# Performance work log

Hardware: AMD Instinct MI355X
Metric: run time of the kernel (lower is better)

Reference implementation:

```python
import jax, jax.numpy as jnp
import numpy as np

R = 32          # voxel_resolution
GN_GROUPS = 8   # GroupNorm groups used throughout the module


def group_norm(x, scale, bias, groups, eps=1e-5):
    B, C = x.shape[0], x.shape[1]
    spatial = x.shape[2:]
    xg = x.reshape(B, groups, C // groups, -1)
    mu = xg.mean(axis=(2, 3), keepdims=True)
    var = xg.var(axis=(2, 3), keepdims=True)
    xn = ((xg - mu) / jnp.sqrt(var + eps)).reshape((B, C) + spatial)
    sh = (1, C) + (1,) * len(spatial)
    return xn * scale.reshape(sh) + bias.reshape(sh)


def conv3d_same(x, w, b):
    pad = w.shape[-1] // 2
    y = jax.lax.conv_general_dilated(
        x, w, (1, 1, 1), [(pad, pad)] * 3,
        dimension_numbers=('NCDHW', 'OIDHW', 'NCDHW'))
    return y + b.reshape(1, -1, 1, 1, 1)


def _voxelize(coords, features, r):
    # PVCNN Voxelization: center coords, normalize to [0,1], scale to grid,
    # scatter-MEAN point features into a dense [B,C,r,r,r] grid.
    B, C, N = features.shape
    centered = coords - coords.mean(axis=2, keepdims=True)            # [B,3,N]
    norm = jnp.linalg.norm(centered, axis=1, keepdims=True)           # [B,1,N]
    denom = norm.max(axis=2, keepdims=True) * 2.0                     # eps = 0
    nc = centered / denom + 0.5
    nc = jnp.clip(nc * r, 0.0, r - 1.0)                               # float voxel coords
    vi = jnp.round(nc).astype(jnp.int32)                              # [B,3,N]
    flat = (vi[:, 0] * r + vi[:, 1]) * r + vi[:, 2]                   # [B,N]
    seg = (flat + (jnp.arange(B, dtype=jnp.int32) * (r ** 3))[:, None]).reshape(-1)
    feats = features.transpose(0, 2, 1).reshape(B * N, C)
    sums = jax.ops.segment_sum(feats, seg, num_segments=B * r ** 3)
    cnts = jax.ops.segment_sum(jnp.ones((B * N,), feats.dtype), seg,
                               num_segments=B * r ** 3)
    mean = sums / jnp.maximum(cnts, 1.0)[:, None]
    grid = mean.reshape(B, r, r, r, C).transpose(0, 4, 1, 2, 3)       # [B,C,r,r,r]
    return nc, grid


def _trilinear_devoxelize(nc, grid, r):
    # nc [B,3,N] float in [0,r-1]; grid [B,C,r,r,r] -> gather 8 corners + weights
    B, C = grid.shape[0], grid.shape[1]
    lo = jnp.floor(nc)
    frac = nc - lo                                                    # [B,3,N]
    lo_i = lo.astype(jnp.int32)
    hi_i = jnp.minimum(lo_i + 1, r - 1)
    gf = grid.reshape(B, C, r * r * r)
    out = jnp.zeros((B, C, nc.shape[2]), grid.dtype)
    for dx in (0, 1):
        for dy in (0, 1):
            for dz in (0, 1):
                ix = hi_i[:, 0] if dx else lo_i[:, 0]
                iy = hi_i[:, 1] if dy else lo_i[:, 1]
                iz = hi_i[:, 2] if dz else lo_i[:, 2]
                w = ((frac[:, 0] if dx else 1.0 - frac[:, 0]) *
                     (frac[:, 1] if dy else 1.0 - frac[:, 1]) *
                     (frac[:, 2] if dz else 1.0 - frac[:, 2]))        # [B,N]
                idx = (ix * r + iy) * r + iz                          # [B,N]
                g = jnp.take_along_axis(gf, idx[:, None, :], axis=2)  # [B,C,N]
                out = out + g * w[:, None, :]
    return out


def setup_inputs() -> dict:
    key = jax.random.key(0)
    ks = jax.random.split(key, 6)
    B, N, Cin, Cout, K = 4, 65536, 64, 128, 3
    return {
        'coords':   jax.random.normal(ks[0], (B, 3, N), jnp.float32),
        'features': jax.random.normal(ks[1], (B, Cin, N), jnp.float32),
        'conv1_w':  jax.random.normal(ks[2], (Cout, Cin, K, K, K), jnp.float32) * 0.02,
        'conv1_b':  jnp.zeros((Cout,), jnp.float32),
        'gn1_scale': jnp.ones((Cout,), jnp.float32),
        'gn1_bias':  jnp.zeros((Cout,), jnp.float32),
        'conv2_w':  jax.random.normal(ks[3], (Cout, Cout, K, K, K), jnp.float32) * 0.02,
        'conv2_b':  jnp.zeros((Cout,), jnp.float32),
        'gn2_scale': jnp.ones((Cout,), jnp.float32),
        'gn2_bias':  jnp.zeros((Cout,), jnp.float32),
        'point_w':  jax.random.normal(ks[4], (Cout, Cin), jnp.float32) * 0.05,
        'point_b':  jnp.zeros((Cout,), jnp.float32),
        'point_gn_scale': jnp.ones((Cout,), jnp.float32),
        'point_gn_bias':  jnp.zeros((Cout,), jnp.float32),
    }


def reference(coords, features, conv1_w, conv1_b, gn1_scale, gn1_bias,
              conv2_w, conv2_b, gn2_scale, gn2_bias,
              point_w, point_b, point_gn_scale, point_gn_bias):
    nc, grid = _voxelize(coords, features, R)
    # voxel branch: Conv3d -> GN -> SiLU -> (dropout, eval: identity) -> Conv3d -> GN -> SiLU
    h = conv3d_same(grid, conv1_w, conv1_b)
    h = jax.nn.silu(group_norm(h, gn1_scale, gn1_bias, GN_GROUPS))
    h = conv3d_same(h, conv2_w, conv2_b)
    h = jax.nn.silu(group_norm(h, gn2_scale, gn2_bias, GN_GROUPS))
    # point branch: SharedMLP = 1x1 Conv1d -> GN -> SiLU
    p = jnp.einsum('oc,bcn->bon', point_w, features) + point_b[None, :, None]
    p = jax.nn.silu(group_norm(p, point_gn_scale, point_gn_bias, GN_GROUPS))
    vpts = _trilinear_devoxelize(nc, h, R)                            # [B,Cout,N]
    return p + vpts
```

## Files before the change

### kernel.cpp

```cpp
#include <hip/hip_runtime.h>

typedef __attribute__((ext_vector_type(8))) short bf16x8;
typedef __attribute__((ext_vector_type(4))) float f32x4;
typedef __attribute__((ext_vector_type(4))) int i32x4;
typedef __attribute__((ext_vector_type(2))) int i32x2;

#define B_ 4
#define N_ 65536
#define RRR_ 32768
#define PADV_ 39304
#define PPLANE_ 1156

static const size_t OFF_NC     = 0;
static const size_t OFF_VIDX   = 786432;
static const size_t OFF_WT1    = 1048576;
static const size_t OFF_WT2    = 1159168;
static const size_t OFF_C2OUT  = 1380352;
static const size_t OFF_CNT    = 9768960;
static const size_t OFF_GSUM   = 9900032;
static const size_t OFF_GPAD   = 18288640;
static const size_t OFF_ACT1   = 23319552;
static const size_t OFF_GSTATS = 33381376;
static const size_t OFF_BSTATS = 33381568;
static const size_t MEMSET_FLOATS = 33381584 - 9768960;
static const size_t OFF_PBF    = 9900032;

__device__ __forceinline__ ushort f2bf(float x) {
    union { float f; unsigned u; } c; c.f = x;
    unsigned r = c.u + 0x7fffu + ((c.u >> 16) & 1u);
    return (ushort)(r >> 16);
}
__device__ __forceinline__ float bf2f(ushort h) {
    union { unsigned u; float f; } c; c.u = ((unsigned)h) << 16;
    return c.f;
}

__device__ __forceinline__ void gl16(const void* g, void* l) {
    __builtin_amdgcn_global_load_lds(
        (const __attribute__((address_space(1))) unsigned int*)(g),
        (__attribute__((address_space(3))) unsigned int*)(l),
        16, 0, 0);
}

__global__ __launch_bounds__(256) void k_coord_sum(const float* __restrict__ coords,
                                                   float* __restrict__ bstats) {
    int b = blockIdx.y;
    int tid = threadIdx.x;
    const float* cb = coords + (size_t)b * 3 * N_;
    float s0 = 0.f, s1 = 0.f, s2 = 0.f;
    for (int n = blockIdx.x * 256 + tid; n < N_; n += 64 * 256) {
        s0 += cb[n]; s1 += cb[N_ + n]; s2 += cb[2 * N_ + n];
    }
    #pragma unroll
    for (int off = 1; off < 64; off <<= 1) {
        s0 += __shfl_xor(s0, off);
        s1 += __shfl_xor(s1, off);
        s2 += __shfl_xor(s2, off);
    }
    if ((tid & 63) == 0) {
        atomicAdd(&bstats[b * 4 + 0], s0);
        atomicAdd(&bstats[b * 4 + 1], s1);
        atomicAdd(&bstats[b * 4 + 2], s2);
    }
}

__global__ __launch_bounds__(256) void k_coord_max(const float* __restrict__ coords,
                                                   float* __restrict__ bstats) {
    int b = blockIdx.y;
    int tid = threadIdx.x;
    const float invN = 1.0f / (float)N_;
    float m0 = bstats[b * 4 + 0] * invN;
    float m1 = bstats[b * 4 + 1] * invN;
    float m2 = bstats[b * 4 + 2] * invN;
    const float* cb = coords + (size_t)b * 3 * N_;
    float mx = 0.f;
    for (int n = blockIdx.x * 256 + tid; n < N_; n += 64 * 256) {
        float x = cb[n] - m0, y = cb[N_ + n] - m1, z = cb[2 * N_ + n] - m2;
        mx = fmaxf(mx, x * x + y * y + z * z);
    }
    #pragma unroll
    for (int off = 1; off < 64; off <<= 1)
        mx = fmaxf(mx, __shfl_xor(mx, off));
    if ((tid & 63) == 0)
        atomicMax((int*)&bstats[b * 4 + 3], __float_as_int(mx));
}

__global__ __launch_bounds__(256) void k_point_prep(const float* __restrict__ coords,
                                                    const float* __restrict__ bstats,
                                                    float* __restrict__ nc,
                                                    int* __restrict__ vidx,
                                                    float* __restrict__ cnt) {
    int gid = blockIdx.x * 256 + threadIdx.x;
    int b = gid >> 16;
    int n = gid & (N_ - 1);
    const float invN = 1.0f / (float)N_;
    float m[3] = {bstats[b * 4 + 0] * invN, bstats[b * 4 + 1] * invN, bstats[b * 4 + 2] * invN};
    float den = 2.0f * sqrtf(__int_as_float(((const int*)bstats)[b * 4 + 3]));
    const float* cb = coords + (size_t)b * 3 * N_;
    int vi[3];
    #pragma unroll
    for (int d = 0; d < 3; ++d) {
        float cv = cb[(size_t)d * N_ + n];
        float t = (cv - m[d]) / den + 0.5f;
        t *= 32.0f;
        t = fminf(fmaxf(t, 0.0f), 31.0f);
        nc[((size_t)b * 3 + d) * N_ + n] = t;
        vi[d] = (int)rintf(t);
    }
    int flat = (vi[0] * 32 + vi[1]) * 32 + vi[2];
    vidx[(b << 16) + n] = flat;
    atomicAdd(&cnt[(b << 15) + flat], 1.0f);
}

__global__ __launch_bounds__(256) void k_scatter_cl(const float* __restrict__ feats,
                                                    const int* __restrict__ vidx,
                                                    float* __restrict__ gsum) {
    __shared__ float lf[64 * 129];
    __shared__ int sidx[128];
    int tid = threadIdx.x;
    int b = blockIdx.y;
    int n0 = blockIdx.x * 128;
    for (int i = tid; i < 64 * 128; i += 256) {
        int ci = i >> 7, pt = i & 127;
        lf[ci * 129 + pt] = feats[((size_t)(b * 64 + ci)) * N_ + n0 + pt];
    }
    if (tid < 128) sidx[tid] = vidx[(b << 16) + n0 + tid];
    __syncthreads();
    for (int i = tid; i < 64 * 128; i += 256) {
        int ci = i & 63, pt = i >> 6;
        atomicAdd(&gsum[((size_t)(b << 15) + sidx[pt]) * 64 + ci], lf[ci * 129 + pt]);
    }
}

__global__ __launch_bounds__(256) void k_gridmean_cl(const float* __restrict__ gsum,
                                                     const float* __restrict__ cnt,
                                                     ushort* __restrict__ gpad) {
    int idx = blockIdx.x * 256 + threadIdx.x;
    int q = idx & 15;
    int vox = (idx >> 4) & 32767;
    int b = idx >> 19;
    float c = cnt[(b << 15) + vox];
    float inv = 1.0f / fmaxf(c, 1.0f);
    float4 v = *(const float4*)(gsum + (((size_t)(b << 15) + vox) << 6) + q * 4);
    int zz = vox >> 10, yy = (vox >> 5) & 31, xx = vox & 31;
    size_t o = ((size_t)b * PADV_ + (size_t)(zz + 1) * PPLANE_ + (yy + 1) * 34 + (xx + 1)) * 64 + q * 4;
    i32x2 pk;
    ushort* u = (ushort*)&pk;
    u[0] = f2bf(v.x * inv); u[1] = f2bf(v.y * inv);
    u[2] = f2bf(v.z * inv); u[3] = f2bf(v.w * inv);
    *(i32x2*)(gpad + o) = pk;
}

template <int CI>
__global__ __launch_bounds__(256) void k_wtrans(const float* __restrict__ w,
                                                ushort* __restrict__ wt) {
    int idx = blockIdx.x * 256 + threadIdx.x;
    if (idx >= 27 * 128 * CI) return;
    int chin = idx & 31;
    int co = (idx >> 5) & 127;
    int t3 = idx >> 12;
    int tap = t3 % 27;
    int chunk = t3 / 27;
    int ci = chunk * 32 + chin;
    wt[idx] = f2bf(w[((size_t)co * CI + ci) * 27 + tap]);
}

template <int CI, bool PAD_OUT>
__global__ __launch_bounds__(256, 2) void k_conv(const ushort* __restrict__ inp,
                                                 const ushort* __restrict__ wt,
                                                 const float* __restrict__ bias,
                                                 ushort* __restrict__ outp,
                                                 float* __restrict__ gstats,
                                                 int layer) {
    constexpr int NCHUNK = CI / 32;
    __shared__ char lds[65536];
    char* ring = lds + 40960;

    const int bid = blockIdx.x;
    const int wid = (bid & 7) * 128 + (bid >> 3);
    const int yg = wid & 7;
    const int z0 = (wid >> 3) & 31;
    const int b = wid >> 8;
    const int y0 = yg * 4;
    const int tid = threadIdx.x;
    const int w = tid >> 6, l = tid & 63;
    const int lk = l >> 4, lr = l & 15;
    const int wr = w >> 1, wc = w & 1;

    const char* actb = (const char*)(inp + (size_t)b * PADV_ * CI);
    const char* wtb = (const char*)wt;

    int st_glb[10];
    #pragma unroll
    for (int j = 0; j < 10; ++j) {
        int c = j * 64 + (tid >> 2);
        if (c > 611) c = 611;
        int row = c / 34;
        int x = c - row * 34;
        int dz = row / 6, dy = row - dz * 6;
        int gz = z0 + dz, gy = y0 + dy;
        int lq = (tid & 3) ^ ((x >> 1) & 3);
        st_glb[j] = (gz * PPLANE_ + gy * 34 + x) * CI * 2 + lq * 16;
    }
    int bst[2];
    #pragma unroll
    for (int i = 0; i < 2; ++i) {
        int s = tid + i * 256;
        int q = s & 3, co = s >> 2;
        bst[i] = co * 64 + ((q ^ ((co >> 1) & 3)) << 4);
    }
    int aoff[4][3];
    #pragma unroll
    for (int i = 0; i < 4; ++i) {
        int pos = wr * 64 + i * 16 + lr;
        int ly = pos >> 5, x = pos & 31;
        #pragma unroll
        for (int fx = 0; fx < 3; ++fx) {
            int xc = x + fx;
            aoff[i][fx] = (ly * 34 + xc) * 64 + ((lk ^ ((xc >> 1) & 3)) << 4);
        }
    }
    int boff[4];
    #pragma unroll
    for (int n = 0; n < 4; ++n) {
        int co = wc * 64 + n * 16 + lr;
        boff[n] = co * 64 + ((lk ^ ((co >> 1) & 3)) << 4);
    }

    f32x4 acc[4][4];
    #pragma unroll
    for (int i = 0; i < 4; ++i)
        #pragma unroll
        for (int n = 0; n < 4; ++n)
            acc[i][n] = (f32x4){0.f, 0.f, 0.f, 0.f};

    #pragma unroll 1
    for (int chunk = 0; chunk < NCHUNK; ++chunk) {
        const char* srcb = actb + chunk * 64;
        const char* wch = wtb + (size_t)chunk * 27 * 8192;
        #pragma unroll
        for (int j = 0; j < 10; ++j)
            gl16(srcb + st_glb[j], lds + j * 4096 + w * 1024);
        #pragma unroll
        for (int i = 0; i < 2; ++i)
            gl16(wch + bst[i], ring + i * 4096 + w * 1024);
        #pragma unroll
        for (int i = 0; i < 2; ++i)
            gl16(wch + 8192 + bst[i], ring + 8192 + i * 4096 + w * 1024);

        #pragma unroll
        for (int t = 0; t < 27; ++t) {
            __builtin_amdgcn_sched_barrier(0);
            if (t == 26) {
                asm volatile("s_waitcnt vmcnt(0)" ::: "memory");
            } else {
                asm volatile("s_waitcnt vmcnt(2)" ::: "memory");
            }
            __builtin_amdgcn_sched_barrier(0);
            __builtin_amdgcn_s_barrier();
            __builtin_amdgcn_sched_barrier(0);
            const char* rp = ring + (t % 3) * 8192;
            const int fz = t / 9, r9v = t - fz * 9;
            const int fy = r9v / 3, fx = r9v - fy * 3;
            const int drow = (fz * 6 + fy) * 2176;
            bf16x8 af[4], bfr[4];
            #pragma unroll
            for (int i = 0; i < 4; ++i)
                af[i] = *(const bf16x8*)(lds + drow + aoff[i][fx]);
            #pragma unroll
            for (int n = 0; n < 4; ++n)
                bfr[n] = *(const bf16x8*)(rp + boff[n]);
            __builtin_amdgcn_s_setprio(1);
            #pragma unroll
            for (int i = 0; i < 4; ++i)
                #pragma unroll
                for (int n = 0; n < 4; ++n)
                    acc[i][n] = __builtin_amdgcn_mfma_f32_16x16x32_bf16(af[i], bfr[n], acc[i][n], 0, 0, 0);
            __builtin_amdgcn_s_setprio(0);
            __builtin_amdgcn_sched_barrier(0);
            if (t + 2 < 27) {
                const char* wp = wch + (size_t)(t + 2) * 8192;
                char* rw = ring + ((t + 2) % 3) * 8192;
                #pragma unroll
                for (int i = 0; i < 2; ++i)
                    gl16(wp + bst[i], rw + i * 4096 + w * 1024);
            }
            __builtin_amdgcn_sched_barrier(0);
        }
        __builtin_amdgcn_s_barrier();
        __builtin_amdgcn_sched_barrier(0);
    }

    ushort* outs = (ushort*)lds;
    float bb[4];
    #pragma unroll
    for (int n = 0; n < 4; ++n) bb[n] = bias[wc * 64 + n * 16 + lr];
    float sg[4] = {0.f, 0.f, 0.f, 0.f}, sq[4] = {0.f, 0.f, 0.f, 0.f};
    #pragma unroll
    for (int i = 0; i < 4; ++i) {
        int posb = wr * 64 + i * 16 + lk * 4;
        #pragma unroll
        for (int n = 0; n < 4; ++n) {
            int co = wc * 64 + n * 16 + lr;
            #pragma unroll
            for (int r = 0; r < 4; ++r) {
                float v = acc[i][n][r] + bb[n];
                sg[n] += v; sq[n] += v * v;
                outs[(posb + r) * 128 + co] = f2bf(v);
            }
        }
    }
    #pragma unroll
    for (int off = 1; off < 64; off <<= 1) {
        #pragma unroll
        for (int n = 0; n < 4; ++n) {
            sg[n] += __shfl_xor(sg[n], off);
            sq[n] += __shfl_xor(sq[n], off);
        }
    }
    if (l == 0) {
        int gbase = layer * 32 + b * 8 + wc * 4;
        #pragma unroll
        for (int n = 0; n < 4; ++n) {
            atomicAdd(&gstats[(gbase + n) * 2 + 0], sg[n]);
            atomicAdd(&gstats[(gbase + n) * 2 + 1], sq[n]);
        }
    }
    __syncthreads();
    for (int idx = tid; idx < 2048; idx += 256) {
        int pos = idx >> 4, c8 = idx & 15;
        int yy = y0 + (pos >> 5), xx = pos & 31;
        size_t g;
        if (PAD_OUT)
            g = ((size_t)b * PADV_ + (size_t)(z0 + 1) * PPLANE_ + (yy + 1) * 34 + (xx + 1)) * 128 + c8 * 8;
        else
            g = ((size_t)b * RRR_ + z0 * 1024 + yy * 32 + xx) * 128 + c8 * 8;
        *(i32x4*)(outp + g) = *((i32x4*)lds + idx);
    }
}

template <bool PAD>
__global__ __launch_bounds__(256) void k_gn_apply(ushort* __restrict__ x,
                                                  const float* __restrict__ gstats,
                                                  const float* __restrict__ sc,
                                                  const float* __restrict__ bi,
                                                  int layer, float invc) {
    int idx = blockIdx.x * 256 + threadIdx.x;
    int c8 = idx & 15;
    int vox = (idx >> 4) & 32767;
    int b = idx >> 19;
    size_t base;
    if (PAD) {
        int zz = vox >> 10, yy = (vox >> 5) & 31, xx = vox & 31;
        base = ((size_t)b * PADV_ + (size_t)(zz + 1) * PPLANE_ + (yy + 1) * 34 + (xx + 1)) * 128 + c8 * 8;
    } else {
        base = ((size_t)b * RRR_ + vox) * 128 + c8 * 8;
    }
    int g = c8 >> 1;
    float sum = gstats[(layer * 32 + b * 8 + g) * 2 + 0];
    float ssq = gstats[(layer * 32 + b * 8 + g) * 2 + 1];
    float mean = sum * invc;
    float var = ssq * invc - mean * mean;
    float rstd = rsqrtf(var + 1e-5f);
    i32x4 raw = *(i32x4*)(x + base);
    ushort* u = (ushort*)&raw;
    #pragma unroll
    for (int j = 0; j < 8; ++j) {
        int co = c8 * 8 + j;
        float v = bf2f(u[j]);
        v = (v - mean) * rstd * sc[co] + bi[co];
        v = v / (1.f + __expf(-v));
        u[j] = f2bf(v);
    }
    *(i32x4*)(x + base) = raw;
}

__global__ __launch_bounds__(256) void k_point_mlp(const float* __restrict__ feats,
                                                   const float* __restrict__ w,
                                                   const float* __restrict__ pb,
                                                   ushort* __restrict__ pbf,
                                                   float* __restrict__ gstats) {
    __shared__ float wl[64 * 132];
    __shared__ float sred[4][16];
    int tid = threadIdx.x;
    for (int i = tid; i < 128 * 64; i += 256) {
        int o = i >> 6, c = i & 63;
        wl[c * 132 + o] = w[i];
    }
    __syncthreads();
    int gid = blockIdx.x * 256 + tid;
    int b = gid >> 16, n = gid & (N_ - 1);
    const float* fb = feats + (size_t)b * 64 * N_ + n;
    float acc[128];
    #pragma unroll
    for (int o = 0; o < 128; ++o) acc[o] = 0.f;
    for (int c = 0; c < 64; ++c) {
        float f = fb[(size_t)c * N_];
        const float4* wr4 = (const float4*)&wl[c * 132];
        #pragma unroll
        for (int o4 = 0; o4 < 32; ++o4) {
            float4 wv = wr4[o4];
            acc[4 * o4 + 0] = fmaf(f, wv.x, acc[4 * o4 + 0]);
            acc[4 * o4 + 1] = fmaf(f, wv.y, acc[4 * o4 + 1]);
            acc[4 * o4 + 2] = fmaf(f, wv.z, acc[4 * o4 + 2]);
            acc[4 * o4 + 3] = fmaf(f, wv.w, acc[4 * o4 + 3]);
        }
    }
    ushort* ob = pbf + (size_t)b * 128 * N_ + n;
    float sg[8] = {0.f}, sq[8] = {0.f};
    #pragma unroll
    for (int o = 0; o < 128; ++o) {
        float v = acc[o] + pb[o];
        ob[(size_t)o * N_] = f2bf(v);
        sg[o >> 4] += v;
        sq[o >> 4] += v * v;
    }
    #pragma unroll
    for (int off = 1; off < 64; off <<= 1) {
        #pragma unroll
        for (int g = 0; g < 8; ++g) {
            sg[g] += __shfl_xor(sg[g], off);
            sq[g] += __shfl_xor(sq[g], off);
        }
    }
    int wv = tid >> 6, l = tid & 63;
    if (l == 0) {
        #pragma unroll
        for (int g = 0; g < 8; ++g) { sred[wv][g] = sg[g]; sred[wv][8 + g] = sq[g]; }
    }
    __syncthreads();
    if (tid < 16) {
        float v = sred[0][tid] + sred[1][tid] + sred[2][tid] + sred[3][tid];
        int g = tid & 7, part = tid >> 3;
        atomicAdd(&gstats[(64 + b * 8 + g) * 2 + part], v);
    }
}

__global__ __launch_bounds__(256) void k_devox_final(const float* __restrict__ nc,
                                                     const ushort* __restrict__ ht,
                                                     const ushort* __restrict__ pbf,
                                                     const float* __restrict__ gstats,
                                                     const float* __restrict__ scale,
                                                     const float* __restrict__ bias,
                                                     float* __restrict__ out) {
    __shared__ float vp[64][129];
    __shared__ int sidx[64][8];
    __shared__ float swt[64][8];
    int tid = threadIdx.x;
    int blk = blockIdx.x;
    int wid = (blk & 7) * 512 + (blk >> 3);
    int b = wid >> 10;
    int n0 = (wid & 1023) * 64;
    if (tid < 64) {
        int n = n0 + tid;
        float f0 = nc[(size_t)b * 3 * N_ + n];
        float f1 = nc[((size_t)b * 3 + 1) * N_ + n];
        float f2 = nc[((size_t)b * 3 + 2) * N_ + n];
        float l0 = floorf(f0), l1 = floorf(f1), l2 = floorf(f2);
        float r0 = f0 - l0, r1 = f1 - l1, r2 = f2 - l2;
        int i0 = (int)l0, i1 = (int)l1, i2 = (int)l2;
        int h0 = min(i0 + 1, 31), h1 = min(i1 + 1, 31), h2 = min(i2 + 1, 31);
        #pragma unroll
        for (int k = 0; k < 8; ++k) {
            int dx = (k >> 2) & 1, dy = (k >> 1) & 1, dz = k & 1;
            int ix = dx ? h0 : i0, iy = dy ? h1 : i1, iz = dz ? h2 : i2;
            float w = (dx ? r0 : 1.f - r0) * (dy ? r1 : 1.f - r1) * (dz ? r2 : 1.f - r2);
            sidx[tid][k] = (ix * 32 + iy) * 32 + iz;
            swt[tid][k] = w;
        }
    }
    __syncthreads();
    const ushort* hb = ht + (size_t)b * RRR_ * 128;
    for (int t = tid; t < 64 * 16; t += 256) {
        int c8 = t & 15, pt = t >> 4;
        float a[8] = {0.f, 0.f, 0.f, 0.f, 0.f, 0.f, 0.f, 0.f};
        #pragma unroll
        for (int k = 0; k < 8; ++k) {
            i32x4 raw = *(const i32x4*)(hb + (size_t)sidx[pt][k] * 128 + c8 * 8);
            ushort* u = (ushort*)&raw;
            float wk = swt[pt][k];
            #pragma unroll
            for (int j = 0; j < 8; ++j)
                a[j] = fmaf(wk, bf2f(u[j]), a[j]);
        }
        #pragma unroll
        for (int j = 0; j < 8; ++j)
            vp[pt][c8 * 8 + j] = a[j];
    }
    __syncthreads();
    const float invc = 1.0f / (16.0f * (float)N_);
    for (int t = tid; t < 64 * 128; t += 256) {
        int nl = t & 63;
        int c = t >> 6;
        int g = c >> 4;
        float sum = gstats[(64 + b * 8 + g) * 2 + 0];
        float ssq = gstats[(64 + b * 8 + g) * 2 + 1];
        float mean = sum * invc;
        float var = ssq * invc - mean * mean;
        float rstd = rsqrtf(var + 1e-5f);
        size_t o = ((size_t)(b * 128 + c)) * N_ + n0 + nl;
        float v = (bf2f(pbf[o]) - mean) * rstd * scale[c] + bias[c];
        v = v / (1.f + __expf(-v));
        out[o] = v + vp[nl][c];
    }
}

extern "C" void kernel_launch(void* const* d_in, const int* in_sizes, int n_in,
                              void* d_out, int out_size, void* d_ws, size_t ws_size,
                              hipStream_t stream) {
    const float* coords   = (const float*)d_in[0];
    const float* features = (const float*)d_in[1];
    const float* conv1_w  = (const float*)d_in[2];
    const float* conv1_b  = (const float*)d_in[3];
    const float* gn1_s    = (const float*)d_in[4];
    const float* gn1_b    = (const float*)d_in[5];
    const float* conv2_w  = (const float*)d_in[6];
    const float* conv2_b  = (const float*)d_in[7];
    const float* gn2_s    = (const float*)d_in[8];
    const float* gn2_b    = (const float*)d_in[9];
    const float* point_w  = (const float*)d_in[10];
    const float* point_b  = (const float*)d_in[11];
    const float* pgn_s    = (const float*)d_in[12];
    const float* pgn_b    = (const float*)d_in[13];
    float* out = (float*)d_out;
    float* ws = (float*)d_ws;

    float*  nc     = ws + OFF_NC;
    int*    vidx   = (int*)(ws + OFF_VIDX);
    ushort* wt1    = (ushort*)(ws + OFF_WT1);
    ushort* wt2    = (ushort*)(ws + OFF_WT2);
    ushort* c2out  = (ushort*)(ws + OFF_C2OUT);
    float*  cnt    = ws + OFF_CNT;
    float*  gsum   = ws + OFF_GSUM;
    ushort* gpad   = (ushort*)(ws + OFF_GPAD);
    ushort* act1   = (ushort*)(ws + OFF_ACT1);
    float*  gstats = ws + OFF_GSTATS;
    float*  bstats = ws + OFF_BSTATS;
    ushort* pbf    = (ushort*)(ws + OFF_PBF);

    const float invc = 1.0f / (float)(RRR_ * 16);

    hipMemsetAsync(cnt, 0, MEMSET_FLOATS * sizeof(float), stream);

    k_coord_sum<<<dim3(64, B_), 256, 0, stream>>>(coords, bstats);
    k_coord_max<<<dim3(64, B_), 256, 0, stream>>>(coords, bstats);
    k_point_prep<<<B_ * N_ / 256, 256, 0, stream>>>(coords, bstats, nc, vidx, cnt);
    k_scatter_cl<<<dim3(N_ / 128, B_), 256, 0, stream>>>(features, vidx, gsum);
    k_gridmean_cl<<<B_ * RRR_ * 16 / 256, 256, 0, stream>>>(gsum, cnt, gpad);

    k_wtrans<64><<<(27 * 128 * 64 + 255) / 256, 256, 0, stream>>>(conv1_w, wt1);
    k_wtrans<128><<<(27 * 128 * 128 + 255) / 256, 256, 0, stream>>>(conv2_w, wt2);

    k_conv<64, true><<<1024, 256, 0, stream>>>(gpad, wt1, conv1_b, act1, gstats, 0);
    k_gn_apply<true><<<B_ * RRR_ * 16 / 256, 256, 0, stream>>>(act1, gstats, gn1_s, gn1_b, 0, invc);

    k_conv<128, false><<<1024, 256, 0, stream>>>(act1, wt2, conv2_b, c2out, gstats, 1);
    k_gn_apply<false><<<B_ * RRR_ * 16 / 256, 256, 0, stream>>>(c2out, gstats, gn2_s, gn2_b, 1, invc);

    k_point_mlp<<<B_ * N_ / 256, 256, 0, stream>>>(features, point_w, point_b, pbf, gstats);
    k_devox_final<<<B_ * N_ / 64, 256, 0, stream>>>(nc, c2out, pbf, gstats, pgn_s, pgn_b, out);
}
```

Baseline: 934.8 us.

## Fuse second GroupNorm+SiLU into devoxelize gather and zero only padding halos

Removes the separate GN2-apply pass over the conv2 output. Each trilinear corner sample is normalized and passed through SiLU inside the devoxelize kernel, using GN2 stats read from gstats. The large memset over the padded grid and activation buffers is replaced by small kernels that zero only the halo voxels, plus a small memset for stats. The fused path recomputes the exp per gathered corner, 8 per point-channel, instead of once per voxel, which trades one memory pass for more ALU work.

```diff
diff --git a/kernel.cpp b/kernel.cpp
--- a/kernel.cpp
+++ b/kernel.cpp
@@ -22,7 +22,7 @@
 static const size_t OFF_ACT1   = 23319552;
 static const size_t OFF_GSTATS = 33381376;
 static const size_t OFF_BSTATS = 33381568;
-static const size_t MEMSET_FLOATS = 33381584 - 9768960;
+static const size_t MEMSET1_FLOATS = 131072 + 8388608;
 static const size_t OFF_PBF    = 9900032;
 
 __device__ __forceinline__ ushort f2bf(float x) {
@@ -40,6 +40,24 @@
         (const __attribute__((address_space(1))) unsigned int*)(g),
         (__attribute__((address_space(3))) unsigned int*)(l),
         16, 0, 0);
+}
+
+template <int CH8>
+__global__ __launch_bounds__(256) void k_zero_halo(ushort* __restrict__ buf) {
+    int idx = blockIdx.x * 256 + threadIdx.x;
+    if (idx >= B_ * PADV_ * CH8) return;
+    int c8 = idx % CH8;
+    int t = idx / CH8;
+    int vox = t % PADV_;
+    int b = t / PADV_;
+    int z = vox / PPLANE_;
+    int rem = vox - z * PPLANE_;
+    int y = rem / 34;
+    int x = rem - y * 34;
+    if (z == 0 || z == 33 || y == 0 || y == 33 || x == 0 || x == 33) {
+        i32x4 zero = (i32x4){0, 0, 0, 0};
+        *(i32x4*)(buf + ((size_t)b * PADV_ + vox) * (CH8 * 8) + c8 * 8) = zero;
+    }
 }
 
 __global__ __launch_bounds__(256) void k_coord_sum(const float* __restrict__ coords,
@@ -440,17 +458,21 @@
                                                      const ushort* __restrict__ ht,
                                                      const ushort* __restrict__ pbf,
                                                      const float* __restrict__ gstats,
+                                                     const float* __restrict__ sc2,
+                                                     const float* __restrict__ bi2,
                                                      const float* __restrict__ scale,
                                                      const float* __restrict__ bias,
                                                      float* __restrict__ out) {
     __shared__ float vp[64][129];
     __shared__ int sidx[64][8];
     __shared__ float swt[64][8];
+    __shared__ float s_sc[128], s_bi[128];
     int tid = threadIdx.x;
     int blk = blockIdx.x;
     int wid = (blk & 7) * 512 + (blk >> 3);
     int b = wid >> 10;
     int n0 = (wid & 1023) * 64;
+    if (tid < 128) { s_sc[tid] = sc2[tid]; s_bi[tid] = bi2[tid]; }
     if (tid < 64) {
         int n = n0 + tid;
         float f0 = nc[(size_t)b * 3 * N_ + n];
@@ -470,9 +492,23 @@
         }
     }
     __syncthreads();
+    const float invcv = 1.0f / (float)(RRR_ * 16);
     const ushort* hb = ht + (size_t)b * RRR_ * 128;
     for (int t = tid; t < 64 * 16; t += 256) {
         int c8 = t & 15, pt = t >> 4;
+        int g2 = c8 >> 1;
+        float sum2 = gstats[(32 + b * 8 + g2) * 2 + 0];
+        float ssq2 = gstats[(32 + b * 8 + g2) * 2 + 1];
+        float mean2 = sum2 * invcv;
+        float var2 = ssq2 * invcv - mean2 * mean2;
+        float rstd2 = rsqrtf(var2 + 1e-5f);
+        float ca[8], cb2[8];
+        #pragma unroll
+        for (int j = 0; j < 8; ++j) {
+            float s = s_sc[c8 * 8 + j] * rstd2;
+            ca[j] = s;
+            cb2[j] = s_bi[c8 * 8 + j] - mean2 * s;
+        }
         float a[8] = {0.f, 0.f, 0.f, 0.f, 0.f, 0.f, 0.f, 0.f};
         #pragma unroll
         for (int k = 0; k < 8; ++k) {
@@ -480,8 +516,11 @@
             ushort* u = (ushort*)&raw;
             float wk = swt[pt][k];
             #pragma unroll
-            for (int j = 0; j < 8; ++j)
-                a[j] = fmaf(wk, bf2f(u[j]), a[j]);
+            for (int j = 0; j < 8; ++j) {
+                float v = fmaf(bf2f(u[j]), ca[j], cb2[j]);
+                v = v / (1.f + __expf(-v));
+                a[j] = fmaf(wk, v, a[j]);
+            }
         }
         #pragma unroll
         for (int j = 0; j < 8; ++j)
@@ -540,7 +579,10 @@
 
     const float invc = 1.0f / (float)(RRR_ * 16);
 
-    hipMemsetAsync(cnt, 0, MEMSET_FLOATS * sizeof(float), stream);
+    hipMemsetAsync(cnt, 0, MEMSET1_FLOATS * sizeof(float), stream);
+    hipMemsetAsync(gstats, 0, (192 + 16) * sizeof(float), stream);
+    k_zero_halo<8><<<(B_ * PADV_ * 8 + 255) / 256, 256, 0, stream>>>(gpad);
+    k_zero_halo<16><<<(B_ * PADV_ * 16 + 255) / 256, 256, 0, stream>>>(act1);
 
     k_coord_sum<<<dim3(64, B_), 256, 0, stream>>>(coords, bstats);
     k_coord_max<<<dim3(64, B_), 256, 0, stream>>>(coords, bstats);
@@ -555,8 +597,8 @@
     k_gn_apply<true><<<B_ * RRR_ * 16 / 256, 256, 0, stream>>>(act1, gstats, gn1_s, gn1_b, 0, invc);
 
     k_conv<128, false><<<1024, 256, 0, stream>>>(act1, wt2, conv2_b, c2out, gstats, 1);
-    k_gn_apply<false><<<B_ * RRR_ * 16 / 256, 256, 0, stream>>>(c2out, gstats, gn2_s, gn2_b, 1, invc);
 
     k_point_mlp<<<B_ * N_ / 256, 256, 0, stream>>>(features, point_w, point_b, pbf, gstats);
-    k_devox_final<<<B_ * N_ / 64, 256, 0, stream>>>(nc, c2out, pbf, gstats, pgn_s, pgn_b, out);
-}
+    k_devox_final<<<B_ * N_ / 64, 256, 0, stream>>>(nc, c2out, pbf, gstats,
+                                                    gn2_s, gn2_b, pgn_s, pgn_b, out);
+}
```

Result: slower. 999.3 us (+6.9%).
